# Kernel optimization log

Measured on AMD Instinct MI355X. Metric: run time of the kernel, lower is better.

## Reference

```python
import jax, jax.numpy as jnp
import numpy as np

N_NODES = 10000
IN_FEATS = 50
HIDDEN = 512
OUT_FEATS = 121
N_EDGES = 160000


def setup_inputs() -> dict:
    key = jax.random.key(0)
    ks = jax.random.split(key, 8)
    x = jax.random.normal(ks[0], (N_NODES, IN_FEATS), dtype=jnp.float32)
    edge_index = jax.random.randint(ks[1], (2, N_EDGES), 0, N_NODES, dtype=jnp.int64)
    # SAGEConv params: lin_l applied to aggregated neighbors (carries bias), lin_r to self.
    def glorot(k, fan_in, fan_out):
        s = jnp.sqrt(6.0 / (fan_in + fan_out))
        return jax.random.uniform(k, (fan_in, fan_out), minval=-s, maxval=s, dtype=jnp.float32)
    W1_l = glorot(ks[2], IN_FEATS, HIDDEN)
    W1_r = glorot(ks[3], IN_FEATS, HIDDEN)
    b1 = jnp.zeros((HIDDEN,), dtype=jnp.float32)
    W2_l = glorot(ks[4], HIDDEN, OUT_FEATS)
    W2_r = glorot(ks[5], HIDDEN, OUT_FEATS)
    b2 = jnp.zeros((OUT_FEATS,), dtype=jnp.float32)
    return {"x": x, "edge_index": edge_index, "W1_l": W1_l, "W1_r": W1_r,
            "b1": b1, "W2_l": W2_l, "W2_r": W2_r, "b2": b2}


def _mean_agg(h, src, dst, n_nodes):
    # gather source features per edge, segment-sum at destination, divide by in-degree
    summed = jax.ops.segment_sum(h[src], dst, num_segments=n_nodes)  # [N, F]
    deg = jax.ops.segment_sum(jnp.ones((src.shape[0],), h.dtype), dst, num_segments=n_nodes)
    return summed / jnp.maximum(deg, 1.0)[:, None]


def _sage_conv(h, src, dst, W_l, W_r, b, n_nodes):
    agg = _mean_agg(h, src, dst, n_nodes)
    return agg @ W_l + h @ W_r + b


def reference(x, edge_index, W1_l, W1_r, b1, W2_l, W2_r, b2):
    src, dst = edge_index[0], edge_index[1]
    n = x.shape[0]
    h = _sage_conv(x, src, dst, W1_l, W1_r, b1, n)
    h = jax.nn.relu(h)
    # dropout is identity in eval mode
    out = _sage_conv(h, src, dst, W2_l, W2_r, b2, n)
    return out
```

## Files before the change

kernel.cpp:

```cpp
#include <hip/hip_runtime.h>
#include <hip/hip_bf16.h>

constexpr int NN   = 10000;
constexpr int INF  = 50;
constexpr int HID  = 512;
constexpr int OUTF = 121;
constexpr int NE   = 160000;
constexpr int DMAX = 64;

typedef __attribute__((ext_vector_type(8))) short short8;
typedef __attribute__((ext_vector_type(4))) float floatx4;

__device__ inline float bf2f(unsigned short u) {
    union { unsigned int i; float f; } v; v.i = ((unsigned)u) << 16; return v.f;
}


__global__ __launch_bounds__(256) void k_prep(const float* __restrict__ x,
                                              const float* __restrict__ W1l, const float* __restrict__ W1r,
                                              const float* __restrict__ W2l, const float* __restrict__ W2r,
                                              int* __restrict__ cursor, __hip_bfloat16* __restrict__ xp,
                                              __hip_bfloat16* __restrict__ A1,
                                              __hip_bfloat16* __restrict__ B1p, __hip_bfloat16* __restrict__ B2p) {
    int idx = blockIdx.x * 256 + threadIdx.x;
    if (idx < NN) cursor[idx] = 0;
    if (idx < 65536) {
        int j = idx & 7, L = (idx >> 3) & 63, kt = (idx >> 9) & 3, nt = idx >> 11;
        int k = kt * 32 + ((L >> 4) * 8 + j);
        int n = nt * 16 + (L & 15);
        float v = (k < 50) ? W1l[k * HID + n] : ((k < 100) ? W1r[(k - 50) * HID + n] : 0.f);
        B1p[idx] = __float2bfloat16(v);
    }
    {
        int j = idx & 7, L = (idx >> 3) & 63, kt = (idx >> 9) & 15, nt = idx >> 13;
        int k = kt * 32 + ((L >> 4) * 8 + j);
        int n = nt * 16 + (L & 15);
        float v;
        if (n < 128) v = (n < OUTF) ? W2l[k * OUTF + n] : 0.f;
        else { int c = n - 128; v = (c < OUTF) ? W2r[k * OUTF + c] : 0.f; }
        B2p[idx] = __float2bfloat16(v);
    }
    for (int r = idx; r < NN * 64; r += 131072) {
        int n = r >> 6, c = r & 63;
        xp[r] = __float2bfloat16(c < INF ? x[n * INF + c] : 0.f);
    }
    for (int r = idx; r < NN * 128; r += 131072) {
        int c = r & 127;
        if (c >= 50) {
            int n = r >> 7;
            A1[r] = __float2bfloat16(c < 100 ? x[n * INF + (c - 50)] : 0.f);
        }
    }
}


__global__ __launch_bounds__(256) void k_fill(const int* __restrict__ srcv, const int* __restrict__ dstv,
                                              int* __restrict__ cursor, int* __restrict__ csr) {
    int e = blockIdx.x * 256 + threadIdx.x;
    if (e < NE) {
        int d = dstv[e];
        if ((unsigned)d < (unsigned)NN) {
            int pos = atomicAdd(&cursor[d], 1);
            int s = srcv[e];
            s = min(max(s, 0), NN - 1);
            if (pos < DMAX) csr[d * DMAX + pos] = s;
        }
    }
}


__global__ __launch_bounds__(256) void k_agg1(const __hip_bfloat16* __restrict__ xp,
                                              const int* __restrict__ cursor, const int* __restrict__ csr,
                                              __hip_bfloat16* __restrict__ A1) {
    int lane = threadIdx.x & 63;
    int n = blockIdx.x * 4 + (threadIdx.x >> 6);
    int dt = cursor[n];
    int d = min(dt, DMAX);
    int ids = csr[n * DMAX + lane];
    const unsigned short* xs = (const unsigned short*)xp;
    float s0 = 0.f, s1 = 0.f, s2 = 0.f, s3 = 0.f;
    int j = 0;
    for (; j + 4 <= d; j += 4) {
        int a = __shfl(ids, j), b = __shfl(ids, j + 1), c = __shfl(ids, j + 2), e = __shfl(ids, j + 3);
        s0 += bf2f(xs[a * 64 + lane]);
        s1 += bf2f(xs[b * 64 + lane]);
        s2 += bf2f(xs[c * 64 + lane]);
        s3 += bf2f(xs[e * 64 + lane]);
    }
    for (; j < d; ++j) {
        int a = __shfl(ids, j);
        s0 += bf2f(xs[a * 64 + lane]);
    }
    float s = (s0 + s1) + (s2 + s3);
    float invd = (dt > 0) ? 1.f / (float)dt : 1.f;
    if (lane < INF) A1[n * 128 + lane] = __float2bfloat16(s * invd);
}


__global__ __launch_bounds__(256) void k_gemm1(const __hip_bfloat16* __restrict__ A1,
                                               const __hip_bfloat16* __restrict__ B1p,
                                               const float* __restrict__ b1,
                                               __hip_bfloat16* __restrict__ h) {
    int t = threadIdx.x;
    int wave = t >> 6, lane = t & 63;
    int quad = lane >> 4, l16 = lane & 15;
    int m0 = blockIdx.x * 16;
    int n0 = blockIdx.y * 256 + wave * 64;

    const short* Arow = (const short*)A1 + (m0 + l16) * 128 + quad * 8;
    short8 af[4];
#pragma unroll
    for (int ks = 0; ks < 4; ++ks) af[ks] = *(const short8*)(Arow + ks * 32);

    floatx4 acc[4];
#pragma unroll
    for (int nt = 0; nt < 4; ++nt) acc[nt] = floatx4{0.f, 0.f, 0.f, 0.f};

#pragma unroll
    for (int nt = 0; nt < 4; ++nt) {
        int ntile = (n0 >> 4) + nt;
        const short* Bb = (const short*)B1p + ((ntile * 4) * 64 + lane) * 8;
#pragma unroll
        for (int ks = 0; ks < 4; ++ks) {
            short8 bf = *(const short8*)(Bb + ks * 512);
            acc[nt] = __builtin_amdgcn_mfma_f32_16x16x32_bf16(af[ks], bf, acc[nt], 0, 0, 0);
        }
    }

#pragma unroll
    for (int nt = 0; nt < 4; ++nt) {
        int col = n0 + nt * 16 + l16;
        float bias = b1[col];
#pragma unroll
        for (int r = 0; r < 4; ++r) {
            int row = m0 + quad * 4 + r;
            float v = fmaxf(acc[nt][r] + bias, 0.f);
            h[row * HID + col] = __float2bfloat16(v);
        }
    }
}


__global__ __launch_bounds__(256) void k_gemm2(const __hip_bfloat16* __restrict__ h,
                                               const __hip_bfloat16* __restrict__ B2p,
                                               __hip_bfloat16* __restrict__ Pb,
                                               float* __restrict__ Q) {
    int t = threadIdx.x;
    int wave = t >> 6, lane = t & 63;
    int quad = lane >> 4, l16 = lane & 15;
    int m0 = blockIdx.x * 16;
    int nloc = wave * 32;
    int nt0 = (blockIdx.y * 128 + nloc) >> 4;

    const short* Arow = (const short*)h + (m0 + l16) * HID + quad * 8;
    const short* B0 = (const short*)B2p + ((nt0 * 16) * 64 + lane) * 8;
    const short* B1 = (const short*)B2p + (((nt0 + 1) * 16) * 64 + lane) * 8;

    floatx4 acc0 = {0.f, 0.f, 0.f, 0.f};
    floatx4 acc1 = {0.f, 0.f, 0.f, 0.f};

#pragma unroll 4
    for (int ks = 0; ks < 16; ++ks) {
        short8 af = *(const short8*)(Arow + ks * 32);
        short8 bf0 = *(const short8*)(B0 + ks * 512);
        short8 bf1 = *(const short8*)(B1 + ks * 512);
        acc0 = __builtin_amdgcn_mfma_f32_16x16x32_bf16(af, bf0, acc0, 0, 0, 0);
        acc1 = __builtin_amdgcn_mfma_f32_16x16x32_bf16(af, bf1, acc1, 0, 0, 0);
    }

    if (blockIdx.y == 0) {
#pragma unroll
        for (int r = 0; r < 4; ++r) {
            int row = m0 + quad * 4 + r;
            Pb[row * 128 + nloc + l16]      = __float2bfloat16(acc0[r]);
            Pb[row * 128 + nloc + 16 + l16] = __float2bfloat16(acc1[r]);
        }
    } else {
#pragma unroll
        for (int r = 0; r < 4; ++r) {
            int row = m0 + quad * 4 + r;
            Q[row * 128 + nloc + l16]      = acc0[r];
            Q[row * 128 + nloc + 16 + l16] = acc1[r];
        }
    }
}


__global__ __launch_bounds__(256) void k_final(const __hip_bfloat16* __restrict__ Pb,
                                               const float* __restrict__ Q, const float* __restrict__ b2,
                                               const int* __restrict__ cursor, const int* __restrict__ csr,
                                               float* __restrict__ out) {
    int lane = threadIdx.x & 63;
    int n = blockIdx.x * 4 + (threadIdx.x >> 6);
    int dt = cursor[n];
    int d = min(dt, DMAX);
    int ids = csr[n * DMAX + lane];
    const unsigned* Pw = (const unsigned*)Pb;
    float lo0 = 0.f, lo1 = 0.f, lo2 = 0.f, lo3 = 0.f;
    float hi0 = 0.f, hi1 = 0.f, hi2 = 0.f, hi3 = 0.f;
    int j = 0;
    for (; j + 4 <= d; j += 4) {
        int a = __shfl(ids, j), b = __shfl(ids, j + 1), c = __shfl(ids, j + 2), e = __shfl(ids, j + 3);
        unsigned w0 = Pw[a * 64 + lane];
        unsigned w1 = Pw[b * 64 + lane];
        unsigned w2 = Pw[c * 64 + lane];
        unsigned w3 = Pw[e * 64 + lane];
        lo0 += __uint_as_float(w0 << 16); hi0 += __uint_as_float(w0 & 0xffff0000u);
        lo1 += __uint_as_float(w1 << 16); hi1 += __uint_as_float(w1 & 0xffff0000u);
        lo2 += __uint_as_float(w2 << 16); hi2 += __uint_as_float(w2 & 0xffff0000u);
        lo3 += __uint_as_float(w3 << 16); hi3 += __uint_as_float(w3 & 0xffff0000u);
    }
    for (; j < d; ++j) {
        int a = __shfl(ids, j);
        unsigned w0 = Pw[a * 64 + lane];
        lo0 += __uint_as_float(w0 << 16); hi0 += __uint_as_float(w0 & 0xffff0000u);
    }
    float slo = (lo0 + lo1) + (lo2 + lo3);
    float shi = (hi0 + hi1) + (hi2 + hi3);
    float invd = (dt > 0) ? 1.f / (float)dt : 1.f;
    int c0 = lane * 2, c1 = lane * 2 + 1;
    if (c0 < OUTF) out[n * OUTF + c0] = slo * invd + Q[n * 128 + c0] + b2[c0];
    if (c1 < OUTF) out[n * OUTF + c1] = shi * invd + Q[n * 128 + c1] + b2[c1];
}

extern "C" void kernel_launch(void* const* d_in, const int* in_sizes, int n_in,
                              void* d_out, int out_size, void* d_ws, size_t ws_size,
                              hipStream_t stream) {
    const float* x   = (const float*)d_in[0];
    const int* edges = (const int*)d_in[1];
    const float* W1l = (const float*)d_in[2];
    const float* W1r = (const float*)d_in[3];
    const float* b1  = (const float*)d_in[4];
    const float* W2l = (const float*)d_in[5];
    const float* W2r = (const float*)d_in[6];
    const float* b2  = (const float*)d_in[7];
    float* out = (float*)d_out;

    char* ws = (char*)d_ws;
    int* cursor         = (int*)(ws + 0);
    int* csr            = (int*)(ws + 40000);
    __hip_bfloat16* xp  = (__hip_bfloat16*)(ws + 2600000);
    __hip_bfloat16* A1  = (__hip_bfloat16*)(ws + 3880000);
    __hip_bfloat16* h   = (__hip_bfloat16*)(ws + 6440000);
    __hip_bfloat16* Pb  = (__hip_bfloat16*)(ws + 16680000);
    float* Q            = (float*)(ws + 19240000);
    __hip_bfloat16* B1p = (__hip_bfloat16*)(ws + 24360000);
    __hip_bfloat16* B2p = (__hip_bfloat16*)(ws + 24491072);

    const int* srcv = edges;
    const int* dstv = edges + NE;

    k_prep<<<512, 256, 0, stream>>>(x, W1l, W1r, W2l, W2r, cursor, xp, A1, B1p, B2p);
    k_fill<<<625, 256, 0, stream>>>(srcv, dstv, cursor, csr);
    k_agg1<<<2500, 256, 0, stream>>>(xp, cursor, csr, A1);
    k_gemm1<<<dim3(625, 2), 256, 0, stream>>>(A1, B1p, b1, h);
    k_gemm2<<<dim3(625, 2), 256, 0, stream>>>(h, B2p, Pb, Q);
    k_final<<<2500, 256, 0, stream>>>(Pb, Q, b2, cursor, csr, out);
}
```

Baseline: 132.5 us.

## Fuse layer-1 aggregation, GEMM1 and GEMM2 into one kernel via LDS

Merges the neighbor-mean aggregation, the first SAGE GEMM with bias+ReLU, and the second-layer projection GEMM into a single kernel per 16-row tile. The aggregated and self features and the hidden activations stay in shared memory, so the A1 and h intermediates no longer round-trip through global memory and two launches disappear. In exchange there are only 625 blocks, each doing serial aggregation for 16 nodes before the MFMA work, which lowers parallelism and occupancy during the gather phase.

```diff
diff --git a/kernel.cpp b/kernel.cpp
--- a/kernel.cpp
+++ b/kernel.cpp
@@ -14,13 +14,16 @@
 __device__ inline float bf2f(unsigned short u) {
     union { unsigned int i; float f; } v; v.i = ((unsigned)u) << 16; return v.f;
 }
+__device__ inline unsigned short f2bf(float f) {
+    __hip_bfloat16 h = __float2bfloat16(f);
+    return *(unsigned short*)&h;
+}
 
 
 __global__ __launch_bounds__(256) void k_prep(const float* __restrict__ x,
                                               const float* __restrict__ W1l, const float* __restrict__ W1r,
                                               const float* __restrict__ W2l, const float* __restrict__ W2r,
                                               int* __restrict__ cursor, __hip_bfloat16* __restrict__ xp,
-                                              __hip_bfloat16* __restrict__ A1,
                                               __hip_bfloat16* __restrict__ B1p, __hip_bfloat16* __restrict__ B2p) {
     int idx = blockIdx.x * 256 + threadIdx.x;
     if (idx < NN) cursor[idx] = 0;
@@ -43,13 +46,6 @@
     for (int r = idx; r < NN * 64; r += 131072) {
         int n = r >> 6, c = r & 63;
         xp[r] = __float2bfloat16(c < INF ? x[n * INF + c] : 0.f);
-    }
-    for (int r = idx; r < NN * 128; r += 131072) {
-        int c = r & 127;
-        if (c >= 50) {
-            int n = r >> 7;
-            A1[r] = __float2bfloat16(c < 100 ? x[n * INF + (c - 50)] : 0.f);
-        }
     }
 }
 
@@ -69,119 +65,107 @@
 }
 
 
-__global__ __launch_bounds__(256) void k_agg1(const __hip_bfloat16* __restrict__ xp,
-                                              const int* __restrict__ cursor, const int* __restrict__ csr,
-                                              __hip_bfloat16* __restrict__ A1) {
-    int lane = threadIdx.x & 63;
-    int n = blockIdx.x * 4 + (threadIdx.x >> 6);
-    int dt = cursor[n];
-    int d = min(dt, DMAX);
-    int ids = csr[n * DMAX + lane];
-    const unsigned short* xs = (const unsigned short*)xp;
-    float s0 = 0.f, s1 = 0.f, s2 = 0.f, s3 = 0.f;
-    int j = 0;
-    for (; j + 4 <= d; j += 4) {
-        int a = __shfl(ids, j), b = __shfl(ids, j + 1), c = __shfl(ids, j + 2), e = __shfl(ids, j + 3);
-        s0 += bf2f(xs[a * 64 + lane]);
-        s1 += bf2f(xs[b * 64 + lane]);
-        s2 += bf2f(xs[c * 64 + lane]);
-        s3 += bf2f(xs[e * 64 + lane]);
-    }
-    for (; j < d; ++j) {
-        int a = __shfl(ids, j);
-        s0 += bf2f(xs[a * 64 + lane]);
-    }
-    float s = (s0 + s1) + (s2 + s3);
-    float invd = (dt > 0) ? 1.f / (float)dt : 1.f;
-    if (lane < INF) A1[n * 128 + lane] = __float2bfloat16(s * invd);
-}
-
-
-__global__ __launch_bounds__(256) void k_gemm1(const __hip_bfloat16* __restrict__ A1,
+__global__ __launch_bounds__(256) void k_fused(const __hip_bfloat16* __restrict__ xp,
+                                               const int* __restrict__ cursor, const int* __restrict__ csr,
                                                const __hip_bfloat16* __restrict__ B1p,
                                                const float* __restrict__ b1,
-                                               __hip_bfloat16* __restrict__ h) {
+                                               const __hip_bfloat16* __restrict__ B2p,
+                                               __hip_bfloat16* __restrict__ Pb, float* __restrict__ Q) {
+    __shared__ __align__(16) unsigned short As[16 * 136];
+    __shared__ __align__(16) unsigned short Ht[16 * 520];
     int t = threadIdx.x;
-    int wave = t >> 6, lane = t & 63;
-    int quad = lane >> 4, l16 = lane & 15;
+    int w = t >> 6, lane = t & 63, quad = lane >> 4, l16 = lane & 15;
     int m0 = blockIdx.x * 16;
-    int n0 = blockIdx.y * 256 + wave * 64;
-
-    const short* Arow = (const short*)A1 + (m0 + l16) * 128 + quad * 8;
+    const unsigned short* xs = (const unsigned short*)xp;
+
+#pragma unroll
+    for (int p = 0; p < 4; ++p) {
+        int nl = w * 4 + p, n = m0 + nl;
+        int dt = cursor[n];
+        int d = min(dt, DMAX);
+        int ids = csr[n * DMAX + lane];
+        float s0 = 0.f, s1 = 0.f, s2 = 0.f, s3 = 0.f;
+        int j = 0;
+        for (; j + 4 <= d; j += 4) {
+            int a = __shfl(ids, j), b = __shfl(ids, j + 1), c = __shfl(ids, j + 2), e = __shfl(ids, j + 3);
+            s0 += bf2f(xs[a * 64 + lane]);
+            s1 += bf2f(xs[b * 64 + lane]);
+            s2 += bf2f(xs[c * 64 + lane]);
+            s3 += bf2f(xs[e * 64 + lane]);
+        }
+        for (; j < d; ++j) {
+            int a = __shfl(ids, j);
+            s0 += bf2f(xs[a * 64 + lane]);
+        }
+        float s = (s0 + s1) + (s2 + s3);
+        float invd = (dt > 0) ? 1.f / (float)dt : 1.f;
+        unsigned short self = xs[n * 64 + lane];
+        if (lane < INF) As[nl * 136 + lane] = f2bf(s * invd);
+        As[nl * 136 + 50 + lane] = self;
+        if (lane < 7) *(unsigned*)&As[nl * 136 + 114 + 2 * lane] = 0u;
+    }
+    __syncthreads();
+
     short8 af[4];
 #pragma unroll
-    for (int ks = 0; ks < 4; ++ks) af[ks] = *(const short8*)(Arow + ks * 32);
-
+    for (int ks = 0; ks < 4; ++ks) af[ks] = *(const short8*)&As[l16 * 136 + ks * 32 + quad * 8];
+    {
+        floatx4 acc[8];
+#pragma unroll
+        for (int nt = 0; nt < 8; ++nt) acc[nt] = floatx4{0.f, 0.f, 0.f, 0.f};
+#pragma unroll
+        for (int nt = 0; nt < 8; ++nt) {
+            int ntile = w * 8 + nt;
+            const short* Bb = (const short*)B1p + (ntile * 4 * 64 + lane) * 8;
+#pragma unroll
+            for (int ks = 0; ks < 4; ++ks) {
+                short8 bf = *(const short8*)(Bb + ks * 512);
+                acc[nt] = __builtin_amdgcn_mfma_f32_16x16x32_bf16(af[ks], bf, acc[nt], 0, 0, 0);
+            }
+        }
+#pragma unroll
+        for (int nt = 0; nt < 8; ++nt) {
+            int col = w * 128 + nt * 16 + l16;
+            float bias = b1[col];
+#pragma unroll
+            for (int r = 0; r < 4; ++r)
+                Ht[(quad * 4 + r) * 520 + col] = f2bf(fmaxf(acc[nt][r] + bias, 0.f));
+        }
+    }
+    __syncthreads();
+
+    int isQ = w >> 1;
+    int halfcol = (w & 1) * 64;
+    int tbase = isQ * 8 + (w & 1) * 4;
     floatx4 acc[4];
 #pragma unroll
     for (int nt = 0; nt < 4; ++nt) acc[nt] = floatx4{0.f, 0.f, 0.f, 0.f};
-
-#pragma unroll
-    for (int nt = 0; nt < 4; ++nt) {
-        int ntile = (n0 >> 4) + nt;
-        const short* Bb = (const short*)B1p + ((ntile * 4) * 64 + lane) * 8;
-#pragma unroll
-        for (int ks = 0; ks < 4; ++ks) {
-            short8 bf = *(const short8*)(Bb + ks * 512);
-            acc[nt] = __builtin_amdgcn_mfma_f32_16x16x32_bf16(af[ks], bf, acc[nt], 0, 0, 0);
-        }
-    }
-
-#pragma unroll
-    for (int nt = 0; nt < 4; ++nt) {
-        int col = n0 + nt * 16 + l16;
-        float bias = b1[col];
-#pragma unroll
-        for (int r = 0; r < 4; ++r) {
-            int row = m0 + quad * 4 + r;
-            float v = fmaxf(acc[nt][r] + bias, 0.f);
-            h[row * HID + col] = __float2bfloat16(v);
-        }
-    }
-}
-
-
-__global__ __launch_bounds__(256) void k_gemm2(const __hip_bfloat16* __restrict__ h,
-                                               const __hip_bfloat16* __restrict__ B2p,
-                                               __hip_bfloat16* __restrict__ Pb,
-                                               float* __restrict__ Q) {
-    int t = threadIdx.x;
-    int wave = t >> 6, lane = t & 63;
-    int quad = lane >> 4, l16 = lane & 15;
-    int m0 = blockIdx.x * 16;
-    int nloc = wave * 32;
-    int nt0 = (blockIdx.y * 128 + nloc) >> 4;
-
-    const short* Arow = (const short*)h + (m0 + l16) * HID + quad * 8;
-    const short* B0 = (const short*)B2p + ((nt0 * 16) * 64 + lane) * 8;
-    const short* B1 = (const short*)B2p + (((nt0 + 1) * 16) * 64 + lane) * 8;
-
-    floatx4 acc0 = {0.f, 0.f, 0.f, 0.f};
-    floatx4 acc1 = {0.f, 0.f, 0.f, 0.f};
-
 #pragma unroll 4
     for (int ks = 0; ks < 16; ++ks) {
-        short8 af = *(const short8*)(Arow + ks * 32);
-        short8 bf0 = *(const short8*)(B0 + ks * 512);
-        short8 bf1 = *(const short8*)(B1 + ks * 512);
-        acc0 = __builtin_amdgcn_mfma_f32_16x16x32_bf16(af, bf0, acc0, 0, 0, 0);
-        acc1 = __builtin_amdgcn_mfma_f32_16x16x32_bf16(af, bf1, acc1, 0, 0, 0);
-    }
-
-    if (blockIdx.y == 0) {
-#pragma unroll
-        for (int r = 0; r < 4; ++r) {
-            int row = m0 + quad * 4 + r;
-            Pb[row * 128 + nloc + l16]      = __float2bfloat16(acc0[r]);
-            Pb[row * 128 + nloc + 16 + l16] = __float2bfloat16(acc1[r]);
-        }
+        short8 a2 = *(const short8*)&Ht[l16 * 520 + ks * 32 + quad * 8];
+#pragma unroll
+        for (int nt = 0; nt < 4; ++nt) {
+            const short* Bb = (const short*)B2p + (((tbase + nt) * 16 + ks) * 64 + lane) * 8;
+            short8 bf = *(const short8*)Bb;
+            acc[nt] = __builtin_amdgcn_mfma_f32_16x16x32_bf16(a2, bf, acc[nt], 0, 0, 0);
+        }
+    }
+    if (!isQ) {
+#pragma unroll
+        for (int nt = 0; nt < 4; ++nt)
+#pragma unroll
+            for (int r = 0; r < 4; ++r) {
+                int row = m0 + quad * 4 + r;
+                Pb[row * 128 + halfcol + nt * 16 + l16] = __float2bfloat16(acc[nt][r]);
+            }
     } else {
 #pragma unroll
-        for (int r = 0; r < 4; ++r) {
-            int row = m0 + quad * 4 + r;
-            Q[row * 128 + nloc + l16]      = acc0[r];
-            Q[row * 128 + nloc + 16 + l16] = acc1[r];
-        }
+        for (int nt = 0; nt < 4; ++nt)
+#pragma unroll
+            for (int r = 0; r < 4; ++r) {
+                int row = m0 + quad * 4 + r;
+                Q[row * 128 + halfcol + nt * 16 + l16] = acc[nt][r];
+            }
     }
 }
 
@@ -240,20 +224,16 @@
     int* cursor         = (int*)(ws + 0);
     int* csr            = (int*)(ws + 40000);
     __hip_bfloat16* xp  = (__hip_bfloat16*)(ws + 2600000);
-    __hip_bfloat16* A1  = (__hip_bfloat16*)(ws + 3880000);
-    __hip_bfloat16* h   = (__hip_bfloat16*)(ws + 6440000);
-    __hip_bfloat16* Pb  = (__hip_bfloat16*)(ws + 16680000);
-    float* Q            = (float*)(ws + 19240000);
-    __hip_bfloat16* B1p = (__hip_bfloat16*)(ws + 24360000);
-    __hip_bfloat16* B2p = (__hip_bfloat16*)(ws + 24491072);
+    __hip_bfloat16* Pb  = (__hip_bfloat16*)(ws + 3880000);
+    float* Q            = (float*)(ws + 6440000);
+    __hip_bfloat16* B1p = (__hip_bfloat16*)(ws + 11560000);
+    __hip_bfloat16* B2p = (__hip_bfloat16*)(ws + 11691072);
 
     const int* srcv = edges;
     const int* dstv = edges + NE;
 
-    k_prep<<<512, 256, 0, stream>>>(x, W1l, W1r, W2l, W2r, cursor, xp, A1, B1p, B2p);
+    k_prep<<<512, 256, 0, stream>>>(x, W1l, W1r, W2l, W2r, cursor, xp, B1p, B2p);
     k_fill<<<625, 256, 0, stream>>>(srcv, dstv, cursor, csr);
-    k_agg1<<<2500, 256, 0, stream>>>(xp, cursor, csr, A1);
-    k_gemm1<<<dim3(625, 2), 256, 0, stream>>>(A1, B1p, b1, h);
-    k_gemm2<<<dim3(625, 2), 256, 0, stream>>>(h, B2p, Pb, Q);
+    k_fused<<<625, 256, 0, stream>>>(xp, cursor, csr, B1p, b1, B2p, Pb, Q);
     k_final<<<2500, 256, 0, stream>>>(Pb, Q, b2, cursor, csr, out);
 }
```

After: 127.4 us. 3.9% less time.
